# Kernel tuning notes

Measured on AMD Instinct MI355X. Metric: run time of the kernel, lower is better.

The kernel has to match this reference:

```python
import jax, jax.numpy as jnp
import numpy as np

G = 8   # channel groups
K = 4   # top-k per group


def setup_inputs() -> dict:
    key = jax.random.key(0)
    ks = jax.random.split(key, 6)
    B, C, H, W = 16, 256, 128, 128
    x = jax.random.normal(ks[0], (B, C, H, W), dtype=jnp.float32)
    # 1x1 conv weights (kernel dims squeezed):
    soft_w1 = jax.random.normal(ks[1], (G, C // G), dtype=jnp.float32) * 0.1  # grouped Conv2d(C, G, 1, groups=G)
    soft_w2 = jax.random.normal(ks[2], (C, G), dtype=jnp.float32) * 0.1       # Conv2d(G, C, 1)
    top_w1 = jax.random.normal(ks[3], (G, K), dtype=jnp.float32) * 0.1        # grouped Conv2d(G*K, G, 1, groups=G)
    top_w2 = jax.random.normal(ks[4], (C, G), dtype=jnp.float32) * 0.1        # Conv2d(G, C, 1)
    r = jax.random.normal(ks[5], (2,), dtype=jnp.float32)                     # branch mixing logits
    return {"x": x, "soft_w1": soft_w1, "soft_w2": soft_w2,
            "top_w1": top_w1, "top_w2": top_w2, "r": r}


def reference(x, soft_w1, soft_w2, top_w1, top_w2, r):
    B, C, H, W = x.shape
    Cg = C // G
    xg = x.reshape(B, G, Cg, H, W)

    # --- CGSoftmax branch: x + conv2(conv1(x * softmax_per_group(x))) ---
    att = jax.nn.softmax(xg, axis=2)          # softmax over within-group channels
    xs = xg * att                              # MulRes
    y = jnp.einsum('bgchw,gc->bghw', xs, soft_w1)     # grouped 1x1 conv C->G
    soft_out = x + jnp.einsum('bghw,og->bohw', y, soft_w2)  # 1x1 conv G->C, AddRes

    # --- CGTopK branch: x + conv2(conv1(topk_per_group(x))) ---
    tk = -jnp.sort(-xg, axis=2)[:, :, :K]      # top-K values, sorted descending: [B,G,K,H,W]
    yt = jnp.einsum('bgkhw,gk->bghw', tk, top_w1)     # grouped 1x1 conv G*K->G
    top_out = x + jnp.einsum('bghw,og->bohw', yt, top_w2)  # 1x1 conv G->C, AddRes

    # --- softmax-weighted branch combine ---
    w = jax.nn.softmax(r)
    rt, rs = w[0], w[1]
    return top_out * rt + soft_out * rs
```

## Files before the change

kernel.cpp:

```cpp
#include <hip/hip_runtime.h>
#include <math.h>


#define G_ 8
#define K_ 4
#define CG_ 32
#define C_ 256
#define HW_ (128 * 128)

__launch_bounds__(512)
__global__ void cgblock_kernel(const float* __restrict__ x,
                               const float* __restrict__ soft_w1,
                               const float* __restrict__ soft_w2,
                               const float* __restrict__ top_w1,
                               const float* __restrict__ top_w2,
                               const float* __restrict__ r,
                               float* __restrict__ out) {
    __shared__ float Ys[G_][64];
    __shared__ float Yt[G_][64];

    const int lane = threadIdx.x & 63;
    const int g = __builtin_amdgcn_readfirstlane(threadIdx.x >> 6);
    const int blk = blockIdx.x;
    const int b = blk >> 8;
    const int s = ((blk & 255) << 6) | lane;

    const int base = (b * C_ + g * CG_) * HW_ + s;
    const float* xp = x + base;

    float v[CG_];
#pragma unroll
    for (int c = 0; c < CG_; ++c) v[c] = xp[c * HW_];

    float m = v[0];
#pragma unroll
    for (int c = 1; c < CG_; ++c) m = fmaxf(m, v[c]);
    float Z = 0.f, acc = 0.f;
#pragma unroll
    for (int c = 0; c < CG_; ++c) {
        float e = __expf(v[c] - m);
        Z += e;
        acc = fmaf(v[c] * e, soft_w1[g * CG_ + c], acc);
    }
    const float ysoft = acc / Z;

    float t0 = -INFINITY, t1 = -INFINITY, t2 = -INFINITY, t3 = -INFINITY;
#pragma unroll
    for (int c = 0; c < CG_; ++c) {
        const float vv = v[c];
        const float c0 = fminf(t0, vv); t0 = fmaxf(t0, vv);
        const float c1 = fminf(t1, c0); t1 = fmaxf(t1, c0);
        const float c2 = fminf(t2, c1); t2 = fmaxf(t2, c1);
        t3 = fmaxf(t3, c2);
    }
    const float ytop = t0 * top_w1[g * K_ + 0] + t1 * top_w1[g * K_ + 1] +
                       t2 * top_w1[g * K_ + 2] + t3 * top_w1[g * K_ + 3];

    Ys[g][lane] = ysoft;
    Yt[g][lane] = ytop;
    __syncthreads();

    const float e0 = __expf(r[0]);
    const float e1 = __expf(r[1]);
    const float rt = e0 / (e0 + e1);
    const float rs = e1 / (e0 + e1);

    float yf[G_], tf[G_];
#pragma unroll
    for (int gg = 0; gg < G_; ++gg) {
        yf[gg] = Ys[gg][lane] * rs;
        tf[gg] = Yt[gg][lane] * rt;
    }

    float* op = out + base;
    const float* w2s = soft_w2 + g * CG_ * G_;
    const float* w2t = top_w2 + g * CG_ * G_;
#pragma unroll
    for (int c = 0; c < CG_; ++c) {
        float o = v[c];
#pragma unroll
        for (int gg = 0; gg < G_; ++gg) {
            o = fmaf(w2s[c * G_ + gg], yf[gg], o);
            o = fmaf(w2t[c * G_ + gg], tf[gg], o);
        }
        op[c * HW_] = o;
    }
}

extern "C" void kernel_launch(void* const* d_in, const int* in_sizes, int n_in,
                              void* d_out, int out_size, void* d_ws, size_t ws_size,
                              hipStream_t stream) {
    const float* x       = (const float*)d_in[0];
    const float* soft_w1 = (const float*)d_in[1];
    const float* soft_w2 = (const float*)d_in[2];
    const float* top_w1  = (const float*)d_in[3];
    const float* top_w2  = (const float*)d_in[4];
    const float* r       = (const float*)d_in[5];
    float* out = (float*)d_out;

    cgblock_kernel<<<dim3(4096), dim3(512), 0, stream>>>(
        x, soft_w1, soft_w2, top_w1, top_w2, r, out);
}
```

Baseline: 447.3 us.

## Process two pixels per thread with float2 nontemporal loads and stores

```diff
diff --git a/kernel.cpp b/kernel.cpp
--- a/kernel.cpp
+++ b/kernel.cpp
@@ -8,6 +8,8 @@
 #define C_ 256
 #define HW_ (128 * 128)
 
+typedef __attribute__((ext_vector_type(2))) float f32x2;
+
 __launch_bounds__(512)
 __global__ void cgblock_kernel(const float* __restrict__ x,
                                const float* __restrict__ soft_w1,
@@ -16,74 +18,98 @@
                                const float* __restrict__ top_w2,
                                const float* __restrict__ r,
                                float* __restrict__ out) {
-    __shared__ float Ys[G_][64];
-    __shared__ float Yt[G_][64];
+    __shared__ f32x2 Ys[G_][64];
+    __shared__ f32x2 Yt[G_][64];
 
     const int lane = threadIdx.x & 63;
     const int g = __builtin_amdgcn_readfirstlane(threadIdx.x >> 6);
     const int blk = blockIdx.x;
-    const int b = blk >> 8;
-    const int s = ((blk & 255) << 6) | lane;
+    const int b = blk >> 7;
+    const int s = ((blk & 127) << 7) | (lane << 1);
 
-    const int base = (b * C_ + g * CG_) * HW_ + s;
-    const float* xp = x + base;
-
-    float v[CG_];
-#pragma unroll
-    for (int c = 0; c < CG_; ++c) v[c] = xp[c * HW_];
-
-    float m = v[0];
-#pragma unroll
-    for (int c = 1; c < CG_; ++c) m = fmaxf(m, v[c]);
-    float Z = 0.f, acc = 0.f;
-#pragma unroll
-    for (int c = 0; c < CG_; ++c) {
-        float e = __expf(v[c] - m);
-        Z += e;
-        acc = fmaf(v[c] * e, soft_w1[g * CG_ + c], acc);
-    }
-    const float ysoft = acc / Z;
-
-    float t0 = -INFINITY, t1 = -INFINITY, t2 = -INFINITY, t3 = -INFINITY;
-#pragma unroll
-    for (int c = 0; c < CG_; ++c) {
-        const float vv = v[c];
-        const float c0 = fminf(t0, vv); t0 = fmaxf(t0, vv);
-        const float c1 = fminf(t1, c0); t1 = fmaxf(t1, c0);
-        const float c2 = fminf(t2, c1); t2 = fmaxf(t2, c1);
-        t3 = fmaxf(t3, c2);
-    }
-    const float ytop = t0 * top_w1[g * K_ + 0] + t1 * top_w1[g * K_ + 1] +
-                       t2 * top_w1[g * K_ + 2] + t3 * top_w1[g * K_ + 3];
-
-    Ys[g][lane] = ysoft;
-    Yt[g][lane] = ytop;
-    __syncthreads();
+    const long base = (long)(b * C_ + g * CG_) * HW_ + s;
+    const f32x2* xp = (const f32x2*)(x + base);
 
     const float e0 = __expf(r[0]);
     const float e1 = __expf(r[1]);
     const float rt = e0 / (e0 + e1);
     const float rs = e1 / (e0 + e1);
 
-    float yf[G_], tf[G_];
+    float va[CG_], vb[CG_];
+#pragma unroll
+    for (int c = 0; c < CG_; ++c) {
+        const f32x2 L = __builtin_nontemporal_load(xp + c * (HW_ / 2));
+        va[c] = L.x;
+        vb[c] = L.y;
+    }
+
+    float ma = va[0], mb = vb[0];
+#pragma unroll
+    for (int c = 1; c < CG_; ++c) {
+        ma = fmaxf(ma, va[c]);
+        mb = fmaxf(mb, vb[c]);
+    }
+    float Za = 0.f, Zb = 0.f, aa = 0.f, ab = 0.f;
+#pragma unroll
+    for (int c = 0; c < CG_; ++c) {
+        const float w1 = soft_w1[g * CG_ + c];
+        const float ea = __expf(va[c] - ma);
+        const float eb = __expf(vb[c] - mb);
+        Za += ea;
+        Zb += eb;
+        aa = fmaf(va[c] * ea, w1, aa);
+        ab = fmaf(vb[c] * eb, w1, ab);
+    }
+    const float ysa = aa / Za;
+    const float ysb = ab / Zb;
+
+    float a0 = -INFINITY, a1 = -INFINITY, a2 = -INFINITY, a3 = -INFINITY;
+    float b0 = -INFINITY, b1 = -INFINITY, b2 = -INFINITY, b3 = -INFINITY;
+#pragma unroll
+    for (int c = 0; c < CG_; ++c) {
+        float u = va[c];
+        float d0 = fminf(a0, u); a0 = fmaxf(a0, u);
+        float d1 = fminf(a1, d0); a1 = fmaxf(a1, d0);
+        float d2 = fminf(a2, d1); a2 = fmaxf(a2, d1);
+        a3 = fmaxf(a3, d2);
+        u = vb[c];
+        d0 = fminf(b0, u); b0 = fmaxf(b0, u);
+        d1 = fminf(b1, d0); b1 = fmaxf(b1, d0);
+        d2 = fminf(b2, d1); b2 = fmaxf(b2, d1);
+        b3 = fmaxf(b3, d2);
+    }
+    const float tw0 = top_w1[g * K_ + 0], tw1 = top_w1[g * K_ + 1];
+    const float tw2 = top_w1[g * K_ + 2], tw3 = top_w1[g * K_ + 3];
+    const float yta = a0 * tw0 + a1 * tw1 + a2 * tw2 + a3 * tw3;
+    const float ytb = b0 * tw0 + b1 * tw1 + b2 * tw2 + b3 * tw3;
+
+    Ys[g][lane] = f32x2{ysa * rs, ysb * rs};
+    Yt[g][lane] = f32x2{yta * rt, ytb * rt};
+    __syncthreads();
+
+    f32x2 yf[G_], tf[G_];
 #pragma unroll
     for (int gg = 0; gg < G_; ++gg) {
-        yf[gg] = Ys[gg][lane] * rs;
-        tf[gg] = Yt[gg][lane] * rt;
+        yf[gg] = Ys[gg][lane];
+        tf[gg] = Yt[gg][lane];
     }
 
-    float* op = out + base;
+    f32x2* op = (f32x2*)(out + base);
     const float* w2s = soft_w2 + g * CG_ * G_;
     const float* w2t = top_w2 + g * CG_ * G_;
 #pragma unroll
     for (int c = 0; c < CG_; ++c) {
-        float o = v[c];
+        float oa = va[c], ob = vb[c];
 #pragma unroll
         for (int gg = 0; gg < G_; ++gg) {
-            o = fmaf(w2s[c * G_ + gg], yf[gg], o);
-            o = fmaf(w2t[c * G_ + gg], tf[gg], o);
+            const float cs = w2s[c * G_ + gg];
+            const float ct = w2t[c * G_ + gg];
+            oa = fmaf(cs, yf[gg].x, oa);
+            ob = fmaf(cs, yf[gg].y, ob);
+            oa = fmaf(ct, tf[gg].x, oa);
+            ob = fmaf(ct, tf[gg].y, ob);
         }
-        op[c * HW_] = o;
+        __builtin_nontemporal_store(f32x2{oa, ob}, op + c * (HW_ / 2));
     }
 }
 
@@ -98,6 +124,6 @@
     const float* r       = (const float*)d_in[5];
     float* out = (float*)d_out;
 
-    cgblock_kernel<<<dim3(4096), dim3(512), 0, stream>>>(
+    cgblock_kernel<<<dim3(2048), dim3(512), 0, stream>>>(
         x, soft_w1, soft_w2, top_w1, top_w2, r, out);
 }
```

New measurement: 438.4 us. 1.02x faster.
